# Performance work log

Hardware: AMD Instinct MI355X
Metric: run time of the kernel (lower is better)

The kernel has to match this reference:

```python
import jax, jax.numpy as jnp
import numpy as np

QMIN, QMAX = 0.0, 255.0  # uint8 activation quantization range


def _qlinear(x, w_q, b, s_in, zp_in, s_w):
    """zentorch_qlinear: quantize fp32 x to uint8, int8 weight, dequant output.

    x:   [M, K] fp32
    w_q: [N, K] int8 values (stored int32), symmetric (weight zp = 0)
    b:   [N] fp32
    s_in, zp_in: scalars (activation scale / zero point)
    s_w: [N] per-output-channel weight scales
    """
    zp = zp_in.astype(jnp.float32)
    q = jnp.clip(jnp.round(x / s_in) + zp, QMIN, QMAX)      # fake-quant uint8
    x_dq = (q - zp) * s_in                                   # dequantized activation
    w_dq = w_q.astype(jnp.float32) * s_w[:, None]            # [N, K] dequant weight
    return x_dq @ w_dq.T + b                                 # [M, N] fp32


def setup_inputs() -> dict:
    key = jax.random.key(0)
    k1, k2, k3, k4 = jax.random.split(key, 4)
    M, K, N = 8192, 4096, 4096
    inp = {
        "input": jax.random.normal(k1, (M, K), dtype=jnp.float32),
        "weights": jax.random.randint(k2, (N, K), -128, 128, dtype=jnp.int32),
        "biases": jax.random.normal(k3, (N,), dtype=jnp.float32) * 0.1,
        "input_scales": jnp.array([0.05], dtype=jnp.float32),
        "input_zero_points": jnp.array([128], dtype=jnp.int32),
        "weight_scales": jax.random.uniform(k4, (N,), dtype=jnp.float32, minval=0.001, maxval=0.01),
        "weight_zero_points": jnp.zeros((N,), dtype=jnp.int32),
        "output_dtype": 0,  # 0 -> float32
    }
    return inp


def reference(input, weights, biases, input_scales, input_zero_points,
              weight_scales, weight_zero_points, output_dtype):
    s_in = input_scales[0]
    zp_in = input_zero_points[0]
    x = _qlinear(input, weights, biases, s_in, zp_in, weight_scales)
    x = _qlinear(x, weights, biases, s_in, zp_in, weight_scales)
    x = _qlinear(x, weights, biases, s_in, zp_in, weight_scales)
    return x
```

## Files before the change

kernel.cpp:

```cpp
#include <hip/hip_runtime.h>
#include <stdint.h>

#define M_DIM 8192
#define K_DIM 4096
#define N_DIM 4096
#define KTILES (K_DIM / 64)

typedef __attribute__((ext_vector_type(4))) int i32x4;

__global__ void pack_w_kernel(const int* __restrict__ w, char* __restrict__ wp,
                              int* __restrict__ corr, const int* __restrict__ zpp) {
  __shared__ int red[256];
  const int n = blockIdx.x;
  const int t = threadIdx.x;
  const int4* row = (const int4*)(w + (size_t)n * K_DIM);
  int s = 0;
  int words[4];
#pragma unroll
  for (int u = 0; u < 4; ++u) {
    int4 v = row[t * 4 + u];
    s += v.x + v.y + v.z + v.w;
    words[u] = (v.x & 255) | ((v.y & 255) << 8) | ((v.z & 255) << 16) | (v.w << 24);
  }
  ((int4*)(wp + (size_t)n * K_DIM))[t] = make_int4(words[0], words[1], words[2], words[3]);
  red[t] = s;
  __syncthreads();
  for (int off = 128; off > 0; off >>= 1) {
    if (t < off) red[t] += red[t + off];
    __syncthreads();
  }
  if (t == 0) corr[n] = (128 - zpp[0]) * red[0];
}

__global__ void quant_in_kernel(const float* __restrict__ x, char* __restrict__ q,
                                const float* __restrict__ sp, const int* __restrict__ zpp) {
  const int i = blockIdx.x * blockDim.x + threadIdx.x;
  const float s = sp[0];
  const float zp = (float)zpp[0];
  float4 v = ((const float4*)x)[i];
  float t0 = fminf(fmaxf(rintf(v.x / s) + zp, 0.f), 255.f);
  float t1 = fminf(fmaxf(rintf(v.y / s) + zp, 0.f), 255.f);
  float t2 = fminf(fmaxf(rintf(v.z / s) + zp, 0.f), 255.f);
  float t3 = fminf(fmaxf(rintf(v.w / s) + zp, 0.f), 255.f);
  int b0 = (int)t0 - 128, b1 = (int)t1 - 128, b2 = (int)t2 - 128, b3 = (int)t3 - 128;
  ((int*)q)[i] = (b0 & 255) | ((b1 & 255) << 8) | ((b2 & 255) << 16) | (b3 << 24);
}

#define STAGE16(SRC, DST)                                                     \
  __builtin_amdgcn_global_load_lds(                                           \
      (const __attribute__((address_space(1))) void*)(SRC),                   \
      (__attribute__((address_space(3))) void*)(DST), 16, 0, 0)

#define RD(p) (*(const i32x4*)(p))

#define TILE_PP(SLOT, KSTG, CA, CB, NA, NB, DO_NEXT)                          \
  {                                                                           \
    const char* bufA_ = &lds[SLOT][0][0];                                     \
    char* nA_ = &lds[((SLOT) + 3) & 3][0][0];                                 \
    char* nB_ = &lds[((SLOT) + 3) & 3][1][0];                                 \
    i32x4 a1_[4];                                                             \
    _Pragma("unroll") for (int i_ = 0; i_ < 4; ++i_)                          \
        a1_[i_] = RD(bufA_ + aoff[4 + i_]);                                   \
    STAGE16(asrc0 + (size_t)(KSTG), nA_ + o0_);                               \
    STAGE16(asrc1 + (size_t)(KSTG), nA_ + o1_);                               \
    __builtin_amdgcn_s_setprio(1);                                            \
    _Pragma("unroll") for (int i_ = 0; i_ < 4; ++i_)                          \
        _Pragma("unroll") for (int j_ = 0; j_ < 4; ++j_)                      \
            acc[i_][j_] = __builtin_amdgcn_mfma_i32_16x16x64_i8(              \
                CA[i_], CB[j_], acc[i_][j_], 0, 0, 0);                        \
    __builtin_amdgcn_s_setprio(0);                                            \
    if (DO_NEXT) {                                                            \
      const char* xA_ = &lds[((SLOT) + 1) & 3][0][0];                         \
      const char* xB_ = &lds[((SLOT) + 1) & 3][1][0];                         \
      _Pragma("unroll") for (int i_ = 0; i_ < 4; ++i_)                        \
          NA[i_] = RD(xA_ + aoff[i_]);                                        \
      _Pragma("unroll") for (int j_ = 0; j_ < 4; ++j_)                        \
          NB[j_] = RD(xB_ + boff[j_]);                                        \
    }                                                                         \
    STAGE16(bsrc0 + (size_t)(KSTG), nB_ + o0_);                               \
    STAGE16(bsrc1 + (size_t)(KSTG), nB_ + o1_);                               \
    __builtin_amdgcn_s_setprio(1);                                            \
    _Pragma("unroll") for (int i_ = 0; i_ < 4; ++i_)                          \
        _Pragma("unroll") for (int j_ = 0; j_ < 4; ++j_)                      \
            acc[4 + i_][j_] = __builtin_amdgcn_mfma_i32_16x16x64_i8(          \
                a1_[i_], CB[j_], acc[4 + i_][j_], 0, 0, 0);                   \
    __builtin_amdgcn_s_setprio(0);                                            \
    asm volatile("s_waitcnt vmcnt(4)" ::: "memory");                          \
    __builtin_amdgcn_s_barrier();                                             \
  }

template <int WRITE_Q>
__global__ __launch_bounds__(512, 2) void gemm_kernel(
    const char* __restrict__ qa, const char* __restrict__ wb,
    const int* __restrict__ corr, const float* __restrict__ swp,
    const float* __restrict__ bias, const float* __restrict__ sp,
    const int* __restrict__ zpp, char* __restrict__ outq, float* __restrict__ outf) {
  __shared__ __align__(16) char lds[4][2][16384];
  const int tid = threadIdx.x;
  const int lane = tid & 63;
  const int w = tid >> 6;
  const int wr = w >> 2;
  const int wc = w & 3;
  const int bid0 = blockIdx.x;
  const int bid = (bid0 & 7) * 64 + (bid0 >> 3);
  const int bm = bid & 31;
  const int bn = bid >> 5;
  const char* abase = qa + (size_t)bm * 256 * K_DIM;
  const char* bbase = wb + (size_t)bn * 256 * K_DIM;

  const int o0_ = tid * 16;
  const int o1_ = 8192 + tid * 16;
  const int r0_ = o0_ >> 6, r1_ = o1_ >> 6;
  const int g0_ = ((o0_ >> 4) & 3) ^ ((r0_ >> 1) & 3);
  const int g1_ = ((o1_ >> 4) & 3) ^ ((r1_ >> 1) & 3);
  const char* asrc0 = abase + (size_t)r0_ * K_DIM + g0_ * 16;
  const char* asrc1 = abase + (size_t)r1_ * K_DIM + g1_ * 16;
  const int p0_ = (r0_ & ~63) + 4 * (r0_ & 15) + ((r0_ >> 4) & 3);
  const int p1_ = (r1_ & ~63) + 4 * (r1_ & 15) + ((r1_ >> 4) & 3);
  const char* bsrc0 = bbase + (size_t)p0_ * K_DIM + g0_ * 16;
  const char* bsrc1 = bbase + (size_t)p1_ * K_DIM + g1_ * 16;

  const int rr = lane & 15;
  const int g = lane >> 4;
  int aoff[8], boff[4];
#pragma unroll
  for (int i = 0; i < 8; ++i) {
    const int row = wr * 128 + i * 16 + rr;
    aoff[i] = (row << 6) + ((g ^ ((row >> 1) & 3)) << 4);
  }
#pragma unroll
  for (int j = 0; j < 4; ++j) {
    const int row = wc * 64 + j * 16 + rr;
    boff[j] = (row << 6) + ((g ^ ((row >> 1) & 3)) << 4);
  }

  i32x4 acc[8][4] = {};

  STAGE16(asrc0, &lds[0][0][o0_]); STAGE16(asrc1, &lds[0][0][o1_]);
  STAGE16(bsrc0, &lds[0][1][o0_]); STAGE16(bsrc1, &lds[0][1][o1_]);
  STAGE16(asrc0 + 64, &lds[1][0][o0_]); STAGE16(asrc1 + 64, &lds[1][0][o1_]);
  STAGE16(bsrc0 + 64, &lds[1][1][o0_]); STAGE16(bsrc1 + 64, &lds[1][1][o1_]);
  STAGE16(asrc0 + 128, &lds[2][0][o0_]); STAGE16(asrc1 + 128, &lds[2][0][o1_]);
  STAGE16(bsrc0 + 128, &lds[2][1][o0_]); STAGE16(bsrc1 + 128, &lds[2][1][o1_]);
  asm volatile("s_waitcnt vmcnt(4)" ::: "memory");
  __builtin_amdgcn_s_barrier();

  i32x4 aA[4], bA[4], aB[4], bB[4];
#pragma unroll
  for (int i = 0; i < 4; ++i) aA[i] = RD(&lds[0][0][0] + aoff[i]);
#pragma unroll
  for (int j = 0; j < 4; ++j) bA[j] = RD(&lds[0][1][0] + boff[j]);

  for (int tb = 0; tb < (KTILES - 4) / 4; ++tb) {
    const int t0 = tb * 4;
    TILE_PP(0, (size_t)(t0 + 3) * 64, aA, bA, aB, bB, 1)
    TILE_PP(1, (size_t)(t0 + 4) * 64, aB, bB, aA, bA, 1)
    TILE_PP(2, (size_t)(t0 + 5) * 64, aA, bA, aB, bB, 1)
    TILE_PP(3, (size_t)(t0 + 6) * 64, aB, bB, aA, bA, 1)
  }
  TILE_PP(0, (size_t)(KTILES - 1) * 64, aA, bA, aB, bB, 1)
  TILE_PP(1, (size_t)(KTILES - 1) * 64, aB, bB, aA, bA, 1)
  TILE_PP(2, (size_t)(KTILES - 1) * 64, aA, bA, aB, bB, 1)
  TILE_PP(3, (size_t)(KTILES - 1) * 64, aB, bB, aA, bA, 0)
  asm volatile("s_waitcnt vmcnt(0)" ::: "memory");

  const float s = sp[0];
  const float zpf = (float)zpp[0];
  const int m0 = bm * 256 + wr * 128 + (lane >> 4) * 4;
  const int nb4 = bn * 256 + wc * 64 + ((lane & 15) << 2);
  const int4 cr4 = *(const int4*)(corr + nb4);
  const float4 sw4 = *(const float4*)(swp + nb4);
  const float4 bb4 = *(const float4*)(bias + nb4);
  const float fs0 = s * sw4.x, fs1 = s * sw4.y, fs2 = s * sw4.z, fs3 = s * sw4.w;
#pragma unroll
  for (int i = 0; i < 8; ++i) {
#pragma unroll
    for (int q = 0; q < 4; ++q) {
      const int m = m0 + i * 16 + q;
      const float v0 = fs0 * (float)(acc[i][0][q] + cr4.x) + bb4.x;
      const float v1 = fs1 * (float)(acc[i][1][q] + cr4.y) + bb4.y;
      const float v2 = fs2 * (float)(acc[i][2][q] + cr4.z) + bb4.z;
      const float v3 = fs3 * (float)(acc[i][3][q] + cr4.w) + bb4.w;
      if (WRITE_Q) {
        const int b0i = (int)fminf(fmaxf(rintf(v0 / s) + zpf, 0.f), 255.f) - 128;
        const int b1i = (int)fminf(fmaxf(rintf(v1 / s) + zpf, 0.f), 255.f) - 128;
        const int b2i = (int)fminf(fmaxf(rintf(v2 / s) + zpf, 0.f), 255.f) - 128;
        const int b3i = (int)fminf(fmaxf(rintf(v3 / s) + zpf, 0.f), 255.f) - 128;
        const uint32_t pk = (uint32_t)(b0i & 255) | ((uint32_t)(b1i & 255) << 8) |
                            ((uint32_t)(b2i & 255) << 16) | ((uint32_t)b3i << 24);
        *(uint32_t*)(outq + (size_t)m * N_DIM + nb4) = pk;
      } else {
        float4 o4;
        o4.x = v0; o4.y = v1; o4.z = v2; o4.w = v3;
        *(float4*)(outf + (size_t)m * N_DIM + nb4) = o4;
      }
    }
  }
}

extern "C" void kernel_launch(void* const* d_in, const int* in_sizes, int n_in,
                              void* d_out, int out_size, void* d_ws, size_t ws_size,
                              hipStream_t stream) {
  const float* x = (const float*)d_in[0];
  const int* wq = (const int*)d_in[1];
  const float* bias = (const float*)d_in[2];
  const float* s_in = (const float*)d_in[3];
  const int* zp_in = (const int*)d_in[4];
  const float* s_w = (const float*)d_in[5];
  float* out = (float*)d_out;

  const size_t WP_BYTES = (size_t)N_DIM * K_DIM;
  const size_t Q_BYTES = (size_t)M_DIM * K_DIM;
  char* ws = (char*)d_ws;
  char* wp = ws;
  char* q1 = ws + WP_BYTES;
  char* q2 = q1 + Q_BYTES;
  int* corr = (int*)(q2 + Q_BYTES);
  const size_t NEEDED = WP_BYTES + 2 * Q_BYTES + (size_t)N_DIM * sizeof(int);
  if (ws_size < NEEDED) return;

  pack_w_kernel<<<N_DIM, 256, 0, stream>>>(wq, wp, corr, zp_in);
  quant_in_kernel<<<(M_DIM * K_DIM / 4) / 256, 256, 0, stream>>>(x, q1, s_in, zp_in);

  dim3 grid((M_DIM / 256) * (N_DIM / 256));
  dim3 blk(512);
  gemm_kernel<1><<<grid, blk, 0, stream>>>(q1, wp, corr, s_w, bias, s_in, zp_in, q2, nullptr);
  gemm_kernel<1><<<grid, blk, 0, stream>>>(q2, wp, corr, s_w, bias, s_in, zp_in, q1, nullptr);
  gemm_kernel<0><<<grid, blk, 0, stream>>>(q1, wp, corr, s_w, bias, s_in, zp_in, nullptr, out);
}
```

Before: 461.5 us.

## Replace 4-stage LDS pipeline with 2-stage double buffer and linear block order

Shrinks the GEMM LDS pipeline from four K-tile stages to two. The kernel now waits for all outstanding global-to-LDS loads (vmcnt(0)) every tile, then reads the next fragments after the barrier instead of prefetching them into registers. It also drops the swizzled block-index remap and uses blockIdx directly. This halves LDS use and fragment registers, but exposes global load latency each iteration and may lose L2 locality between neighbouring blocks.

```diff
diff --git a/kernel.cpp b/kernel.cpp
--- a/kernel.cpp
+++ b/kernel.cpp
@@ -53,40 +53,40 @@
 
 #define RD(p) (*(const i32x4*)(p))
 
-#define TILE_PP(SLOT, KSTG, CA, CB, NA, NB, DO_NEXT)                          \
+#define TILE2(SLOT, KN, DO_NEXT)                                              \
   {                                                                           \
-    const char* bufA_ = &lds[SLOT][0][0];                                     \
-    char* nA_ = &lds[((SLOT) + 3) & 3][0][0];                                 \
-    char* nB_ = &lds[((SLOT) + 3) & 3][1][0];                                 \
+    const char* cA_ = &lds[SLOT][0][0];                                       \
+    char* nA_ = &lds[(SLOT) ^ 1][0][0];                                       \
+    char* nB_ = &lds[(SLOT) ^ 1][1][0];                                       \
     i32x4 a1_[4];                                                             \
     _Pragma("unroll") for (int i_ = 0; i_ < 4; ++i_)                          \
-        a1_[i_] = RD(bufA_ + aoff[4 + i_]);                                   \
-    STAGE16(asrc0 + (size_t)(KSTG), nA_ + o0_);                               \
-    STAGE16(asrc1 + (size_t)(KSTG), nA_ + o1_);                               \
+        a1_[i_] = RD(cA_ + aoff[4 + i_]);                                     \
+    if (DO_NEXT) {                                                            \
+      STAGE16(asrc0 + (size_t)(KN), nA_ + o0_);                               \
+      STAGE16(asrc1 + (size_t)(KN), nA_ + o1_);                               \
+      STAGE16(bsrc0 + (size_t)(KN), nB_ + o0_);                               \
+      STAGE16(bsrc1 + (size_t)(KN), nB_ + o1_);                               \
+    }                                                                         \
     __builtin_amdgcn_s_setprio(1);                                            \
     _Pragma("unroll") for (int i_ = 0; i_ < 4; ++i_)                          \
         _Pragma("unroll") for (int j_ = 0; j_ < 4; ++j_)                      \
             acc[i_][j_] = __builtin_amdgcn_mfma_i32_16x16x64_i8(              \
-                CA[i_], CB[j_], acc[i_][j_], 0, 0, 0);                        \
+                a0[i_], b0[j_], acc[i_][j_], 0, 0, 0);                        \
     __builtin_amdgcn_s_setprio(0);                                            \
-    if (DO_NEXT) {                                                            \
-      const char* xA_ = &lds[((SLOT) + 1) & 3][0][0];                         \
-      const char* xB_ = &lds[((SLOT) + 1) & 3][1][0];                         \
-      _Pragma("unroll") for (int i_ = 0; i_ < 4; ++i_)                        \
-          NA[i_] = RD(xA_ + aoff[i_]);                                        \
-      _Pragma("unroll") for (int j_ = 0; j_ < 4; ++j_)                        \
-          NB[j_] = RD(xB_ + boff[j_]);                                        \
-    }                                                                         \
-    STAGE16(bsrc0 + (size_t)(KSTG), nB_ + o0_);                               \
-    STAGE16(bsrc1 + (size_t)(KSTG), nB_ + o1_);                               \
     __builtin_amdgcn_s_setprio(1);                                            \
     _Pragma("unroll") for (int i_ = 0; i_ < 4; ++i_)                          \
         _Pragma("unroll") for (int j_ = 0; j_ < 4; ++j_)                      \
             acc[4 + i_][j_] = __builtin_amdgcn_mfma_i32_16x16x64_i8(          \
-                a1_[i_], CB[j_], acc[4 + i_][j_], 0, 0, 0);                   \
+                a1_[i_], b0[j_], acc[4 + i_][j_], 0, 0, 0);                   \
     __builtin_amdgcn_s_setprio(0);                                            \
-    asm volatile("s_waitcnt vmcnt(4)" ::: "memory");                          \
+    asm volatile("s_waitcnt vmcnt(0)" ::: "memory");                          \
     __builtin_amdgcn_s_barrier();                                             \
+    if (DO_NEXT) {                                                            \
+      _Pragma("unroll") for (int i_ = 0; i_ < 4; ++i_)                        \
+          a0[i_] = RD(nA_ + aoff[i_]);                                        \
+      _Pragma("unroll") for (int j_ = 0; j_ < 4; ++j_)                        \
+          b0[j_] = RD(nB_ + boff[j_]);                                        \
+    }                                                                         \
   }
 
 template <int WRITE_Q>
@@ -95,14 +95,13 @@
     const int* __restrict__ corr, const float* __restrict__ swp,
     const float* __restrict__ bias, const float* __restrict__ sp,
     const int* __restrict__ zpp, char* __restrict__ outq, float* __restrict__ outf) {
-  __shared__ __align__(16) char lds[4][2][16384];
+  __shared__ __align__(16) char lds[2][2][16384];
   const int tid = threadIdx.x;
   const int lane = tid & 63;
   const int w = tid >> 6;
   const int wr = w >> 2;
   const int wc = w & 3;
-  const int bid0 = blockIdx.x;
-  const int bid = (bid0 & 7) * 64 + (bid0 >> 3);
+  const int bid = blockIdx.x;
   const int bm = bid & 31;
   const int bn = bid >> 5;
   const char* abase = qa + (size_t)bm * 256 * K_DIM;
@@ -138,31 +137,22 @@
 
   STAGE16(asrc0, &lds[0][0][o0_]); STAGE16(asrc1, &lds[0][0][o1_]);
   STAGE16(bsrc0, &lds[0][1][o0_]); STAGE16(bsrc1, &lds[0][1][o1_]);
-  STAGE16(asrc0 + 64, &lds[1][0][o0_]); STAGE16(asrc1 + 64, &lds[1][0][o1_]);
-  STAGE16(bsrc0 + 64, &lds[1][1][o0_]); STAGE16(bsrc1 + 64, &lds[1][1][o1_]);
-  STAGE16(asrc0 + 128, &lds[2][0][o0_]); STAGE16(asrc1 + 128, &lds[2][0][o1_]);
-  STAGE16(bsrc0 + 128, &lds[2][1][o0_]); STAGE16(bsrc1 + 128, &lds[2][1][o1_]);
-  asm volatile("s_waitcnt vmcnt(4)" ::: "memory");
+  asm volatile("s_waitcnt vmcnt(0)" ::: "memory");
   __builtin_amdgcn_s_barrier();
 
-  i32x4 aA[4], bA[4], aB[4], bB[4];
-#pragma unroll
-  for (int i = 0; i < 4; ++i) aA[i] = RD(&lds[0][0][0] + aoff[i]);
-#pragma unroll
-  for (int j = 0; j < 4; ++j) bA[j] = RD(&lds[0][1][0] + boff[j]);
-
-  for (int tb = 0; tb < (KTILES - 4) / 4; ++tb) {
-    const int t0 = tb * 4;
-    TILE_PP(0, (size_t)(t0 + 3) * 64, aA, bA, aB, bB, 1)
-    TILE_PP(1, (size_t)(t0 + 4) * 64, aB, bB, aA, bA, 1)
-    TILE_PP(2, (size_t)(t0 + 5) * 64, aA, bA, aB, bB, 1)
-    TILE_PP(3, (size_t)(t0 + 6) * 64, aB, bB, aA, bA, 1)
-  }
-  TILE_PP(0, (size_t)(KTILES - 1) * 64, aA, bA, aB, bB, 1)
-  TILE_PP(1, (size_t)(KTILES - 1) * 64, aB, bB, aA, bA, 1)
-  TILE_PP(2, (size_t)(KTILES - 1) * 64, aA, bA, aB, bB, 1)
-  TILE_PP(3, (size_t)(KTILES - 1) * 64, aB, bB, aA, bA, 0)
-  asm volatile("s_waitcnt vmcnt(0)" ::: "memory");
+  i32x4 a0[4], b0[4];
+#pragma unroll
+  for (int i = 0; i < 4; ++i) a0[i] = RD(&lds[0][0][0] + aoff[i]);
+#pragma unroll
+  for (int j = 0; j < 4; ++j) b0[j] = RD(&lds[0][1][0] + boff[j]);
+
+  for (int tb = 0; tb < (KTILES - 2) / 2; ++tb) {
+    const size_t k0 = (size_t)(tb * 2 + 1) * 64;
+    TILE2(0, k0, 1)
+    TILE2(1, k0 + 64, 1)
+  }
+  TILE2(0, (size_t)(KTILES - 1) * 64, 1)
+  TILE2(1, 0, 0)
 
   const float s = sp[0];
   const float zpf = (float)zpp[0];
```

New measurement: 453.1 us. No clear change (-1.8%).
